# Optimization experiments

Hardware: AMD Instinct MI355X
Metric: run time of the kernel (lower is better)

The kernel has to match this reference:

```python
import math
import jax, jax.numpy as jnp
import numpy as np

L_LAYERS, H, D, DV, DM, LMAX, V = 4, 16, 1024, 64, 4096, 1024, 32000


def setup_inputs() -> dict:
    key = jax.random.key(0)
    ks = iter(jax.random.split(key, 40))
    def rn(shape, s=0.02):
        return jax.random.normal(next(ks), shape, jnp.float32) * s
    x_ids = jax.random.randint(next(ks), (LMAX,), 0, V)
    return dict(
        x_ids=x_ids,
        word_emb=rn((V, D)), pos_emb=rn((LMAX, D)),
        Wq=rn((L_LAYERS, H, D, D)), bq=jnp.zeros((L_LAYERS, H, D), jnp.float32),
        Wk=rn((L_LAYERS, H, D, D)), bk=jnp.zeros((L_LAYERS, H, D), jnp.float32),
        Wv=rn((L_LAYERS, H, D, DV)), bv=jnp.zeros((L_LAYERS, H, DV), jnp.float32),
        Wo=rn((L_LAYERS, H * DV, D)), bo=jnp.zeros((L_LAYERS, D), jnp.float32),
        g1=rn((L_LAYERS, D), 0.01), b1=rn((L_LAYERS, D), 0.01),
        g2=rn((L_LAYERS, D), 0.01), b2=rn((L_LAYERS, D), 0.01),
        W1=rn((L_LAYERS, D, DM)), bm1=jnp.zeros((L_LAYERS, DM), jnp.float32),
        W2=rn((L_LAYERS, DM, D)), bm2=jnp.zeros((L_LAYERS, D), jnp.float32),
        gf=rn((D,), 0.01), bf=rn((D,), 0.01),
        Wu=rn((D, V)), bu=jnp.zeros((V,), jnp.float32),
    )


def _ln(x, g, b):
    # original normalizes each row over the full embedding vector (biased std)
    mu = jnp.mean(x, axis=-1, keepdims=True)
    sd = jnp.sqrt(jnp.mean((x - mu) ** 2, axis=-1, keepdims=True))
    return g * (x - mu) / sd + b


def reference(x_ids, word_emb, pos_emb, Wq, bq, Wk, bk, Wv, bv, Wo, bo,
              g1, b1, g2, b2, W1, bm1, W2, bm2, gf, bf, Wu, bu):
    x = word_emb[x_ids] + pos_emb[jnp.arange(LMAX)]          # (LMAX, D)
    mask = jnp.tril(jnp.ones((LMAX, LMAX), bool))
    scale = 1.0 / math.sqrt(D)                               # d_attn = d_e
    for l in range(L_LAYERS):
        xn = _ln(x, g1[l], b1[l])
        q = jnp.einsum('ld,hde->hle', xn, Wq[l]) + bq[l][:, None, :]
        k = jnp.einsum('ld,hde->hle', xn, Wk[l]) + bk[l][:, None, :]
        v = jnp.einsum('ld,hdv->hlv', xn, Wv[l]) + bv[l][:, None, :]
        s = jnp.einsum('hqe,hke->hqk', q, k)                 # (H, LMAX, LMAX)
        s = jnp.where(mask, s, -jnp.inf)
        a = jax.nn.softmax(s * scale, axis=-1)
        o = jnp.einsum('hqk,hkv->hqv', a, v)                 # (H, LMAX, DV)
        # faithful reproduction of MHAttention's OVERLAPPING slice writes:
        # head h writes columns [h, h+DV), later heads overwrite earlier ones
        y = jnp.zeros((LMAX, H * DV), x.dtype)
        for h in range(H):
            y = y.at[:, h:h + DV].set(o[h])
        x = x + y @ Wo[l] + bo[l]
        xn2 = _ln(x, g2[l], b2[l])
        # x + act_layer(xn2) where act_layer(z) = z + mlp2(gelu(mlp1(z)))
        x = x + xn2 + jax.nn.gelu(xn2 @ W1[l] + bm1[l]) @ W2[l] + bm2[l]
    x = _ln(x, gf, bf)
    return jax.nn.softmax(x @ Wu + bu, axis=-1)              # (LMAX, V)
```

## Files before the change

### kernel.cpp

```cpp
#include <hip/hip_runtime.h>

typedef __bf16 bf16_t;
typedef __bf16 bf16x8 __attribute__((ext_vector_type(8)));
typedef float f32x4 __attribute__((ext_vector_type(4)));
typedef unsigned int u32;

#define SEQ    1024
#define DEMB   1024
#define NHEAD  16
#define DVDIM  64
#define DMLP   4096
#define NVOCAB 32000
#define NLAYER 4

typedef const __attribute__((address_space(1))) void gas_t;
typedef __attribute__((address_space(3))) void las_t;

__device__ __forceinline__ void gload_lds16(const void* g, void* l) {
  __builtin_amdgcn_global_load_lds((gas_t*)g, (las_t*)l, 16, 0, 0);
}

union PackU { bf16_t h[2]; u32 u; };
union B4U  { uint2 u; bf16_t h[4]; };

__device__ __forceinline__ float blockSum(float v, float* red) {
  #pragma unroll
  for (int o = 32; o > 0; o >>= 1) v += __shfl_down(v, o, 64);
  __syncthreads();
  if ((threadIdx.x & 63) == 0) red[threadIdx.x >> 6] = v;
  __syncthreads();
  return (red[0] + red[1]) + (red[2] + red[3]);
}
__device__ __forceinline__ float blockMax(float v, float* red) {
  #pragma unroll
  for (int o = 32; o > 0; o >>= 1) v = fmaxf(v, __shfl_down(v, o, 64));
  __syncthreads();
  if ((threadIdx.x & 63) == 0) red[threadIdx.x >> 6] = v;
  __syncthreads();
  return fmaxf(fmaxf(red[0], red[1]), fmaxf(red[2], red[3]));
}

__device__ __forceinline__ void ln_body(float4 v, const float* __restrict__ g,
                                        const float* __restrict__ b,
                                        bf16_t* __restrict__ xn, int row, int t,
                                        float* red, float* xupd_row) {
  float mu = blockSum(v.x + v.y + v.z + v.w, red) * (1.0f / DEMB);
  float dx = v.x - mu, dy = v.y - mu, dz = v.z - mu, dw = v.w - mu;
  float var = blockSum(dx * dx + dy * dy + dz * dz + dw * dw, red) * (1.0f / DEMB);
  float inv = 1.0f / sqrtf(var);
  float4 gv = *(const float4*)(g + t * 4);
  float4 bv = *(const float4*)(b + t * 4);
  float o0 = gv.x * dx * inv + bv.x;
  float o1 = gv.y * dy * inv + bv.y;
  float o2 = gv.z * dz * inv + bv.z;
  float o3 = gv.w * dw * inv + bv.w;
  PackU p0, p1;
  p0.h[0] = (bf16_t)o0; p0.h[1] = (bf16_t)o1;
  p1.h[0] = (bf16_t)o2; p1.h[1] = (bf16_t)o3;
  uint2 st; st.x = p0.u; st.y = p1.u;
  *(uint2*)(xn + (long)row * DEMB + t * 4) = st;
  if (xupd_row) {
    float4 nv; nv.x = v.x + o0; nv.y = v.y + o1; nv.z = v.z + o2; nv.w = v.w + o3;
    *(float4*)(xupd_row + t * 4) = nv;
  }
}

__global__ void __launch_bounds__(256)
embedln_k(const int* __restrict__ ids, const float* __restrict__ we,
          const float* __restrict__ pe, const float* __restrict__ g,
          const float* __restrict__ b, float* __restrict__ x,
          bf16_t* __restrict__ xn) {
  __shared__ float red[4];
  const int row = blockIdx.x, t = threadIdx.x;
  const long id = ids[row];
  float4 a = *(const float4*)(we + id * (long)DEMB + t * 4);
  float4 p = *(const float4*)(pe + (long)row * DEMB + t * 4);
  float4 v; v.x = a.x + p.x; v.y = a.y + p.y; v.z = a.z + p.z; v.w = a.w + p.w;
  *(float4*)(x + (long)row * DEMB + t * 4) = v;
  ln_body(v, g, b, xn, row, t, red, nullptr);
}

__global__ void __launch_bounds__(256)
ln_k(const float* __restrict__ x, const float* __restrict__ g,
     const float* __restrict__ b, bf16_t* __restrict__ xn,
     float* __restrict__ xupd) {
  __shared__ float red[4];
  const int row = blockIdx.x, t = threadIdx.x;
  float4 v = *(const float4*)(x + (long)row * DEMB + t * 4);
  ln_body(v, g, b, xn, row, t, red, xupd ? xupd + (long)row * DEMB : nullptr);
}

__global__ void __launch_bounds__(256)
redln_k(const float* __restrict__ P, const float* __restrict__ bm2,
        float* __restrict__ X, const float* __restrict__ g,
        const float* __restrict__ b, bf16_t* __restrict__ xn) {
  __shared__ float red[4];
  const int row = blockIdx.x, t = threadIdx.x;
  const long i = (long)row * 1024 + t * 4;
  float4 x = *(float4*)(X + i);
  #pragma unroll
  for (int z = 0; z < 4; ++z) {
    float4 p = *(const float4*)(P + (long)z * 1048576 + i);
    x.x += p.x; x.y += p.y; x.z += p.z; x.w += p.w;
  }
  float4 bb = *(const float4*)(bm2 + t * 4);
  x.x += bb.x; x.y += bb.y; x.z += bb.z; x.w += bb.w;
  *(float4*)(X + i) = x;
  ln_body(x, g, b, xn, row, t, red, nullptr);
}

__global__ void biaszyb_k(const float* __restrict__ bq, const float* __restrict__ bk,
                          float* __restrict__ out, bf16_t* __restrict__ y) {
  const int z = blockIdx.x, t = threadIdx.x;
  if (z < 128) {
    const int l = z >> 5, i = z & 31;
    const float* src = (i < NHEAD) ? (bq + (long)(l * NHEAD + i) * DEMB)
                                   : (bk + (long)(l * NHEAD + i - NHEAD) * DEMB);
    *(float4*)(out + (long)z * DEMB + t * 4) = *(const float4*)(src + t * 4);
  } else {
    *(uint4*)((char*)y + ((long)(z - 128) * 256 + t) * 16) = uint4{0, 0, 0, 0};
  }
}

__device__ __forceinline__ void tconv_tile(const float* __restrict__ ip,
                                           bf16_t* __restrict__ op,
                                           int R, int C, int rx, int ry,
                                           float (*tf)[65]) {
  const int c0 = rx * 64, r0 = ry * 128;
  const int t = threadIdx.x;
  #pragma unroll
  for (int p = 0; p < 8; ++p) {
    const int i = p * 256 + t;
    const int r = i >> 4, c4 = (i & 15) * 4;
    const float4 v = *(const float4*)(ip + (long)(r0 + r) * C + (c0 + c4));
    *(float4*)&tf[r][c4] = v;
  }
  __syncthreads();
  const int nn = t >> 2;
  const int sub = t & 3;
  #pragma unroll
  for (int q2 = 0; q2 < 4; ++q2) {
    const int base = q2 * 32 + sub * 8;
    u32 w[4];
    #pragma unroll
    for (int q = 0; q < 4; ++q) {
      PackU u;
      u.h[0] = (bf16_t)tf[base + 2 * q][nn];
      u.h[1] = (bf16_t)tf[base + 2 * q + 1][nn];
      w[q] = u.u;
    }
    *(uint4*)(op + (long)(c0 + nn) * R + (r0 + base)) = *(uint4*)&w[0];
  }
}

__global__ void __launch_bounds__(256)
tconvall_k(const float* __restrict__ Wq, const float* __restrict__ Wk,
           const float* __restrict__ Wv, const float* __restrict__ Wo,
           const float* __restrict__ W1, const float* __restrict__ W2,
           const float* __restrict__ Wu,
           bf16_t* __restrict__ WTqk, bf16_t* __restrict__ WTv,
           bf16_t* __restrict__ WTo, bf16_t* __restrict__ WT1,
           bf16_t* __restrict__ WT2, bf16_t* __restrict__ WTu) {
  __shared__ float tf[128][65];
  const long DD = (long)DEMB * DEMB;
  const int b = blockIdx.x;
  const float* ip; bf16_t* op; int R, C, rx, ry;
  if (b < 16384) {
    const int z = b >> 7, rem = b & 127; ry = rem >> 4; rx = rem & 15;
    R = 1024; C = 1024;
    const int l = z >> 5, i = z & 31;
    ip = (i < NHEAD) ? (Wq + (long)(l * NHEAD + i) * DD)
                     : (Wk + (long)(l * NHEAD + i - NHEAD) * DD);
    op = WTqk + (long)z * DD;
  } else if (b < 16896) {
    const int idx = b - 16384; const int z = idx >> 3; ry = idx & 7; rx = 0;
    R = 1024; C = 64;
    ip = Wv + (long)z * 65536; op = WTv + (long)z * 65536;
  } else if (b < 16960) {
    const int idx = b - 16896; const int z = idx >> 4; ry = 0; rx = idx & 15;
    R = 128; C = 1024;
    ip = Wo + (long)z * DD; op = WTo + (long)z * 131072;
  } else if (b < 19008) {
    const int idx = b - 16960; const int z = idx >> 9, rem = idx & 511;
    ry = rem >> 6; rx = rem & 63;
    R = 1024; C = 4096;
    ip = W1 + (long)z * 4194304; op = WT1 + (long)z * 4194304;
  } else if (b < 21056) {
    const int idx = b - 19008; const int z = idx >> 9, rem = idx & 511;
    ry = rem >> 4; rx = rem & 15;
    R = 4096; C = 1024;
    ip = W2 + (long)z * 4194304; op = WT2 + (long)z * 4194304;
  } else {
    const int idx = b - 21056; ry = idx / 500; rx = idx - ry * 500;
    R = 1024; C = 32000;
    ip = Wu; op = WTu;
  }
  tconv_tile(ip, op, R, C, rx, ry, tf);
}

template<int MODE, int BN, bool CAUSAL, bool TRIMK>
__global__ void __launch_bounds__(256)
gemm_k(const bf16_t* __restrict__ A, const bf16_t* __restrict__ B,
       const float* __restrict__ bias, void* __restrict__ Cv,
       int M, int N, int K, int lda, int ldb,
       long aB, long bB, long cB, int biasB) {
  __shared__ bf16_t lsA[128 * 32];
  __shared__ bf16_t lsB[BN * 32];

  const int t = threadIdx.x;
  const int bz = blockIdx.z;
  const int m0 = blockIdx.y * 128;
  const int n0 = blockIdx.x * BN;
  if (CAUSAL && n0 > m0 + 127) return;

  const bf16_t* Ap = A + (long)bz * aB;
  const bf16_t* Bp = B + (long)bz * bB;
  const int kEnd = TRIMK ? min(K, m0 + 128) : K;

  constexpr int NS = BN / 32;
  const int lane = t & 63;
  const int wid = t >> 6;
  const int wr = (wid >> 1) * 64;
  const int wc = (wid & 1) * (BN / 2);
  const int fr = lane & 15, fg = lane >> 4;
  const int srow = lane >> 2;
  const int skc  = (lane & 3) * 8;

  f32x4 acc[4][NS] = {};

  for (int k0 = 0; k0 < kEnd; k0 += 32) {
    if (k0) __syncthreads();
    #pragma unroll
    for (int i = 0; i < 2; ++i) {
      const int seg = wid * 2 + i;
      gload_lds16(Ap + (long)(m0 + seg * 16 + srow) * lda + (k0 + skc),
                  lsA + seg * 512);
    }
    if (BN == 128) {
      #pragma unroll
      for (int i = 0; i < 2; ++i) {
        const int seg = wid * 2 + i;
        gload_lds16(Bp + (long)(n0 + seg * 16 + srow) * ldb + (k0 + skc),
                    lsB + seg * 512);
      }
    } else {
      gload_lds16(Bp + (long)(n0 + wid * 16 + srow) * ldb + (k0 + skc),
                  lsB + wid * 512);
    }
    __syncthreads();

    bf16x8 af[4], bfv[NS];
    #pragma unroll
    for (int ms = 0; ms < 4; ++ms)
      af[ms] = *(const bf16x8*)(lsA + (wr + ms * 16 + fr) * 32 + fg * 8);
    #pragma unroll
    for (int ns = 0; ns < NS; ++ns)
      bfv[ns] = *(const bf16x8*)(lsB + (wc + ns * 16 + fr) * 32 + fg * 8);
    #pragma unroll
    for (int ms = 0; ms < 4; ++ms)
      #pragma unroll
      for (int ns = 0; ns < NS; ++ns)
        acc[ms][ns] = __builtin_amdgcn_mfma_f32_16x16x32_bf16(
            af[ms], bfv[ns], acc[ms][ns], 0, 0, 0);
  }

  #pragma unroll
  for (int ms = 0; ms < 4; ++ms) {
    #pragma unroll
    for (int ns = 0; ns < NS; ++ns) {
      const int col = n0 + wc + ns * 16 + fr;
      const float bvv = bias ? bias[(long)bz * biasB + col] : 0.0f;
      #pragma unroll
      for (int r = 0; r < 4; ++r) {
        const int row = m0 + wr + ms * 16 + fg * 4 + r;
        float v = acc[ms][ns][r] + bvv;
        if (MODE == 1) {
          ((float*)Cv)[(long)bz * cB + (long)row * N + col] += v;
        } else if (MODE == 2) {
          ((float*)Cv)[(long)bz * cB + (long)row * N + col] = v;
        } else {
          float gl = 0.5f * v * (1.0f + tanhf(0.7978845608028654f * (v + 0.044715f * v * v * v)));
          ((bf16_t*)Cv)[(long)bz * cB + (long)row * N + col] = (bf16_t)gl;
        }
      }
    }
  }
}

#define GPHASE(buf, mh, nh, STAGE, VM) do {                                            \
  bf16x8 af[4][2], bfv[2][2];                                                          \
  _Pragma("unroll") for (int mf = 0; mf < 4; ++mf) {                                   \
    const int r = wm * 128 + ((mh) * 4 + mf) * 16 + (lane & 15);                       \
    _Pragma("unroll") for (int ks = 0; ks < 2; ++ks) {                                 \
      const int slot = ks * 4 + (lane >> 4);                                           \
      af[mf][ks] = *(const bf16x8*)(lds + (buf) * 32768 + r * 64 +                     \
                                    ((slot ^ (r & 7)) << 3)); } }                      \
  _Pragma("unroll") for (int nf = 0; nf < 2; ++nf) {                                   \
    const int r = wn * 64 + ((nh) * 2 + nf) * 16 + (lane & 15);                        \
    _Pragma("unroll") for (int ks = 0; ks < 2; ++ks) {                                 \
      const int slot = ks * 4 + (lane >> 4);                                           \
      bfv[nf][ks] = *(const bf16x8*)(lds + (buf) * 32768 + 16384 + r * 64 +            \
                                     ((slot ^ (r & 7)) << 3)); } }                     \
  STAGE;                                                                               \
  __builtin_amdgcn_s_barrier();                                                        \
  asm volatile("s_waitcnt lgkmcnt(0)" ::: "memory");                                   \
  __builtin_amdgcn_sched_barrier(0);                                                   \
  __builtin_amdgcn_s_setprio(1);                                                       \
  _Pragma("unroll") for (int mf = 0; mf < 4; ++mf)                                     \
    _Pragma("unroll") for (int nf = 0; nf < 2; ++nf)                                   \
      _Pragma("unroll") for (int ks = 0; ks < 2; ++ks)                                 \
        acc[(mh) * 4 + mf][(nh) * 2 + nf] = __builtin_amdgcn_mfma_f32_16x16x32_bf16(   \
            af[mf][ks], bfv[nf][ks], acc[(mh) * 4 + mf][(nh) * 2 + nf], 0, 0, 0);      \
  __builtin_amdgcn_s_setprio(0);                                                       \
  VM;                                                                                  \
  __builtin_amdgcn_s_barrier();                                                        \
} while (0)

template<int MODE, bool CAUSAL, int VZ, bool PACKED>
__global__ void __launch_bounds__(512, 1)
gemm256_k(const bf16_t* __restrict__ A, const bf16_t* __restrict__ B,
          const float* __restrict__ bias, void* __restrict__ Cv,
          int M, int N, int K, long aB, long bB, long cB, int biasB,
          const bf16_t* __restrict__ A2, const bf16_t* __restrict__ B2,
          const float* __restrict__ bias2, bf16_t* __restrict__ Cv2) {
  __shared__ bf16_t lds[65536];

  const int t = threadIdx.x;
  const int lane = t & 63, w = t >> 6;
  const int wm = w >> 2, wn = w & 3;
  int m0, n0, zz; bool vm;
  if (PACKED) {
    const int id = blockIdx.x;
    if (id < 16) {
      vm = true; zz = 0;
      m0 = (id >> 2) * 256; n0 = (id & 3) * 256;
    } else {
      vm = false;
      const int idd = id - 16;
      zz = idd & 15;
      const int pi = idd >> 4;
      const int by = (pi >= 1) + (pi >= 3) + (pi >= 6);
      const int bx = pi - (by * (by + 1)) / 2;
      m0 = by * 256; n0 = bx * 256;
    }
  } else {
    zz = blockIdx.z; m0 = blockIdx.y * 256; n0 = blockIdx.x * 256;
    vm = (VZ >= 0) && (zz == VZ);
    if (CAUSAL && !vm && n0 > m0 + 255) return;
  }

  const bf16_t* Ap = vm ? A2 : A + (long)zz * aB;
  const bf16_t* Bp = vm ? B2 : B + (long)zz * bB;
  const int NT = K >> 6;

  f32x4 acc[8][4] = {};

  auto stA = [&](int half, int kt, int buf) {
    #pragma unroll
    for (int rr = 0; rr < 2; ++rr) {
      const int rw0 = rr * 64 + w * 8;
      const int row0 = ((rw0 >> 6) << 7) | (half << 6) | (rw0 & 63);
      const int r = row0 + (lane >> 3);
      const int slot = lane & 7;
      gload_lds16(Ap + (long)(m0 + r) * K + (kt << 6) + ((slot ^ (r & 7)) << 3),
                  lds + buf * 32768 + row0 * 64);
    }
  };
  auto stB = [&](int half, int kt, int buf) {
    #pragma unroll
    for (int rr = 0; rr < 2; ++rr) {
      const int rw0 = rr * 64 + w * 8;
      const int row0 = ((rw0 >> 5) << 6) | (half << 5) | (rw0 & 31);
      const int r = row0 + (lane >> 3);
      const int slot = lane & 7;
      gload_lds16(Bp + (long)(n0 + r) * K + (kt << 6) + ((slot ^ (r & 7)) << 3),
                  lds + buf * 32768 + 16384 + row0 * 64);
    }
  };

  stB(0, 0, 0); stA(0, 0, 0); stA(1, 0, 0); stB(1, 0, 0);
  stB(0, 1, 1); stA(0, 1, 1);
  asm volatile("s_waitcnt vmcnt(4)" ::: "memory");
  __builtin_amdgcn_s_barrier();

  for (int it = 0; it < (NT >> 1); ++it) {
    const int tt = it * 2;
    const int s1 = min(tt + 1, NT - 1);
    const int s2 = min(tt + 2, NT - 1);
    const int s3 = min(tt + 3, NT - 1);
    GPHASE(0, 0, 0, { stA(1, s1, 1); }, );
    GPHASE(0, 1, 0, { stB(1, s1, 1); }, );
    GPHASE(0, 0, 1, { stB(0, s2, 0); }, );
    GPHASE(0, 1, 1, { stA(0, s2, 0); }, asm volatile("s_waitcnt vmcnt(4)" ::: "memory"));
    GPHASE(1, 0, 0, { stA(1, s2, 0); }, );
    GPHASE(1, 1, 0, { stB(1, s2, 0); }, );
    GPHASE(1, 0, 1, { stB(0, s3, 1); }, );
    GPHASE(1, 1, 1, { stA(0, s3, 1); }, asm volatile("s_waitcnt vmcnt(4)" ::: "memory"));
  }
  asm volatile("s_waitcnt vmcnt(0)" ::: "memory");

  #pragma unroll
  for (int mf = 0; mf < 8; ++mf) {
    #pragma unroll
    for (int nf = 0; nf < 4; ++nf) {
      const int col = n0 + wn * 64 + nf * 16 + (lane & 15);
      const int row0 = m0 + wm * 128 + mf * 16 + (lane >> 4) * 4;
      if (vm) {
        const float bvv = bias2[col];
        PackU p0, p1;
        p0.h[0] = (bf16_t)(acc[mf][nf][0] + bvv);
        p0.h[1] = (bf16_t)(acc[mf][nf][1] + bvv);
        p1.h[0] = (bf16_t)(acc[mf][nf][2] + bvv);
        p1.h[1] = (bf16_t)(acc[mf][nf][3] + bvv);
        uint2 st; st.x = p0.u; st.y = p1.u;
        *(uint2*)(Cv2 + (long)col * M + row0) = st;
      } else {
        const float bvv = bias ? bias[(long)zz * biasB + col] : 0.0f;
        #pragma unroll
        for (int r = 0; r < 4; ++r) {
          const float v = acc[mf][nf][r] + bvv;
          if (MODE == 0)
            ((bf16_t*)Cv)[(long)zz * cB + (long)(row0 + r) * N + col] = (bf16_t)v;
          else
            ((float*)Cv)[(long)zz * cB + (long)(row0 + r) * N + col] = v;
        }
      }
    }
  }
}

__global__ void __launch_bounds__(256)
smax_k(const bf16_t* __restrict__ s, const bf16_t* __restrict__ V,
       bf16_t* __restrict__ Yb) {
  __shared__ float pl[4][1024];
  const int qb = blockIdx.x, h = blockIdx.y, t = threadIdx.x;
  const int w = t >> 6, lane = t & 63;
  const int q = qb * 4 + w;
  const bf16_t* sr = s + ((long)h * SEQ + q) * SEQ;
  const int L = q + 1;
  const float scale = 0.03125f;
  float e[16];
  float m = -1e30f;
  #pragma unroll
  for (int c = 0; c < 4; ++c) {
    B4U bb; bb.u = *(const uint2*)(sr + lane * 16 + c * 4);
    #pragma unroll
    for (int j = 0; j < 4; ++j) {
      const float x = (float)bb.h[j] * scale;
      e[c * 4 + j] = x;
      if (lane * 16 + c * 4 + j < L) m = fmaxf(m, x);
    }
  }
  #pragma unroll
  for (int o = 32; o > 0; o >>= 1) m = fmaxf(m, __shfl_xor(m, o, 64));
  float sum = 0.0f;
  #pragma unroll
  for (int i = 0; i < 16; ++i) {
    e[i] = (lane * 16 + i < L) ? expf(e[i] - m) : 0.0f;
    sum += e[i];
  }
  #pragma unroll
  for (int o = 32; o > 0; o >>= 1) sum += __shfl_xor(sum, o, 64);
  const float inv = 1.0f / sum;

  if (h != NHEAD - 1) {
    const bf16_t* vc = V + (long)h * 64 * SEQ + lane * 16;
    float d = 0.0f;
    #pragma unroll
    for (int c = 0; c < 4; ++c) {
      B4U vv; vv.u = *(const uint2*)(vc + c * 4);
      #pragma unroll
      for (int j = 0; j < 4; ++j) d += e[c * 4 + j] * (float)vv.h[j];
    }
    #pragma unroll
    for (int o = 32; o > 0; o >>= 1) d += __shfl_xor(d, o, 64);
    if (lane == 0) Yb[(long)q * 128 + h] = (bf16_t)(d * inv);
  } else {
    #pragma unroll
    for (int c = 0; c < 4; ++c)
      *(float4*)&pl[w][lane * 16 + c * 4] = *(float4*)&e[c * 4];
    __syncthreads();
    const int c = t & 63, r = t >> 6;
    const int qq = qb * 4 + r;
    const bf16_t* vr = V + ((long)(NHEAD - 1) * 64 + c) * SEQ;
    float d = 0.0f;
    for (int kk = 0; kk < 1024; kk += 8) {
      bf16x8 v8 = *(const bf16x8*)(vr + kk);
      #pragma unroll
      for (int j = 0; j < 8; ++j) d += pl[r][kk + j] * (float)v8[j];
    }
    float sr2 = 0.0f;
    for (int kk = t & 63; kk < 1024; kk += 64) sr2 += pl[r][kk];
    #pragma unroll
    for (int o = 32; o > 0; o >>= 1) sr2 += __shfl_xor(sr2, o, 64);
    Yb[(long)qq * 128 + 15 + c] = (bf16_t)(d / sr2);
  }
}

__global__ void __launch_bounds__(1024)
vsmax_k(float* __restrict__ out) {
  __shared__ float rm[16], rs[16];
  const int row = blockIdx.x, t = threadIdx.x;
  float* r = out + (long)row * NVOCAB;
  float v[32];
  const int nlast = (t < NVOCAB - 31 * 1024) ? 32 : 31;
  float m = -1e30f;
  #pragma unroll
  for (int j = 0; j < 31; ++j) { v[j] = r[j * 1024 + t]; m = fmaxf(m, v[j]); }
  if (nlast == 32) { v[31] = r[31 * 1024 + t]; m = fmaxf(m, v[31]); } else v[31] = -1e30f;
  float s = 0.0f;
  #pragma unroll
  for (int j = 0; j < 32; ++j) s += expf(v[j] - m);
  #pragma unroll
  for (int o = 32; o > 0; o >>= 1) {
    const float mo = __shfl_down(m, o, 64);
    const float so = __shfl_down(s, o, 64);
    const float M2 = fmaxf(m, mo);
    s = s * expf(m - M2) + so * expf(mo - M2);
    m = M2;
  }
  if ((t & 63) == 0) { rm[t >> 6] = m; rs[t >> 6] = s; }
  __syncthreads();
  float M = -1e30f;
  #pragma unroll
  for (int i = 0; i < 16; ++i) M = fmaxf(M, rm[i]);
  float S = 0.0f;
  #pragma unroll
  for (int i = 0; i < 16; ++i) S += rs[i] * expf(rm[i] - M);
  const float inv = 1.0f / S;
  #pragma unroll
  for (int j = 0; j < 31; ++j) r[j * 1024 + t] = expf(v[j] - M) * inv;
  if (nlast == 32) r[31 * 1024 + t] = expf(v[31] - M) * inv;
}

extern "C" void kernel_launch(void* const* d_in, const int* in_sizes, int n_in,
                              void* d_out, int out_size, void* d_ws, size_t ws_size,
                              hipStream_t stream) {
  (void)in_sizes; (void)n_in; (void)out_size; (void)ws_size;
  const int*   x_ids = (const int*)  d_in[0];
  const float* wemb  = (const float*)d_in[1];
  const float* pemb  = (const float*)d_in[2];
  const float* Wq    = (const float*)d_in[3];
  const float* bq    = (const float*)d_in[4];
  const float* Wk    = (const float*)d_in[5];
  const float* bk    = (const float*)d_in[6];
  const float* Wv    = (const float*)d_in[7];
  const float* bv    = (const float*)d_in[8];
  const float* Wo    = (const float*)d_in[9];
  const float* bo    = (const float*)d_in[10];
  const float* g1    = (const float*)d_in[11];
  const float* b1    = (const float*)d_in[12];
  const float* g2    = (const float*)d_in[13];
  const float* b2    = (const float*)d_in[14];
  const float* W1    = (const float*)d_in[15];
  const float* bm1   = (const float*)d_in[16];
  const float* W2    = (const float*)d_in[17];
  const float* bm2   = (const float*)d_in[18];
  const float* gf    = (const float*)d_in[19];
  const float* bfin  = (const float*)d_in[20];
  const float* Wu    = (const float*)d_in[21];
  const float* bu    = (const float*)d_in[22];

  char* ws = (char*)d_ws;
  float*  X    = (float*) ws;
  bf16_t* ACT  = (bf16_t*)(ws + (4u   << 20));
  bf16_t* VbT  = (bf16_t*)(ws + (6u   << 20));
  bf16_t* Yb   = (bf16_t*)(ws + (10u  << 20));
  bf16_t* H1   = (bf16_t*)(ws + (12u  << 20));
  bf16_t* QKb  = (bf16_t*)(ws + (20u  << 20));
  float*  PART = (float*) (ws + (84u  << 20));
  float*  BIAS = (float*) (ws + (100u << 20));
  bf16_t* WTqk = (bf16_t*)(ws + (128u << 20));
  bf16_t* WTv  = (bf16_t*)(ws + (384u << 20));
  bf16_t* WTo  = (bf16_t*)(ws + (392u << 20));
  bf16_t* WT1  = (bf16_t*)(ws + (400u << 20));
  bf16_t* WT2  = (bf16_t*)(ws + (432u << 20));
  bf16_t* WTu  = (bf16_t*)(ws + (464u << 20));

  bf16_t* Sb  = (bf16_t*)d_out;
  float*  OUT = (float*)d_out;

  const long DD = (long)DEMB * DEMB;
  const long SD = (long)SEQ * DEMB;

  embedln_k<<<SEQ, 256, 0, stream>>>(x_ids, wemb, pemb, g1, b1, X, ACT);
  biaszyb_k<<<192, 256, 0, stream>>>(bq, bk, BIAS, Yb);
  tconvall_k<<<25056, 256, 0, stream>>>(Wq, Wk, Wv, Wo, W1, W2, Wu,
                                        WTqk, WTv, WTo, WT1, WT2, WTu);

  for (int l = 0; l < NLAYER; ++l) {
    gemm256_k<0, false, -1, false><<<dim3(4, 4, 32), 512, 0, stream>>>(
        ACT, WTqk + (long)l * 32 * DD, BIAS + (long)l * 32 * DEMB, QKb,
        SEQ, DEMB, DEMB, 0L, DD, SD, DEMB,
        nullptr, nullptr, nullptr, nullptr);

    gemm256_k<0, true, 0, true><<<dim3(176), 512, 0, stream>>>(
        QKb, QKb + (long)NHEAD * SD, nullptr, Sb,
        SEQ, SEQ, DEMB, SD, SD, (long)SEQ * SEQ, 0,
        ACT, WTv + (long)l * DD, bv + (long)l * NHEAD * DVDIM, VbT);

    smax_k<<<dim3(SEQ / 4, NHEAD), 256, 0, stream>>>(Sb, VbT, Yb);

    gemm_k<1, 64, false, false><<<dim3(16, 8, 1), 256, 0, stream>>>(
        Yb, WTo + (long)l * DEMB * 128, bo + (long)l * DEMB, X,
        SEQ, DEMB, 128, 128, 128, 0L, 0L, 0L, 0);

    ln_k<<<SEQ, 256, 0, stream>>>(X, g2 + l * DEMB, b2 + l * DEMB, ACT, X);

    gemm_k<3, 128, false, false><<<dim3(32, 8, 1), 256, 0, stream>>>(
        ACT, WT1 + (long)l * DMLP * DEMB, bm1 + (long)l * DMLP, H1,
        SEQ, DMLP, DEMB, DEMB, DEMB, 0L, 0L, 0L, 0);
    gemm_k<2, 128, false, false><<<dim3(8, 8, 4), 256, 0, stream>>>(
        H1, WT2 + (long)l * DEMB * DMLP, nullptr, PART,
        SEQ, DEMB, 1024, DMLP, DMLP, 1024L, 1024L, (long)SEQ * DEMB, 0);
    if (l < NLAYER - 1)
      redln_k<<<SEQ, 256, 0, stream>>>(PART, bm2 + (long)l * DEMB, X,
                                       g1 + (l + 1) * DEMB, b1 + (l + 1) * DEMB, ACT);
    else
      redln_k<<<SEQ, 256, 0, stream>>>(PART, bm2 + (long)l * DEMB, X, gf, bfin, ACT);
  }

  gemm256_k<2, false, -1, false><<<dim3(125, 4, 1), 512, 0, stream>>>(
      ACT, WTu, bu, OUT, SEQ, NVOCAB, DEMB, 0L, 0L, 0L, 0,
      nullptr, nullptr, nullptr, nullptr);
  vsmax_k<<<SEQ, 1024, 0, stream>>>(OUT);
}
```

Baseline: 1.393 ms.

## Write bf16 logits to workspace, fuse init kernels, nontemporal weight-transpose stores

The vocab GEMM now writes bf16 logits into a scratch region (reusing the QK weight area) instead of fp32 into the output. The softmax kernel reads these bf16 pairs and writes fp32 probabilities as float2, which halves the logit write and read traffic. The embedding/LN kernel absorbs the bias-copy and zero-fill kernel, saving one launch. Weight-transpose stores become nontemporal. Rounding logits to bf16 before the softmax adds precision error.

```diff
diff --git a/kernel.cpp b/kernel.cpp
--- a/kernel.cpp
+++ b/kernel.cpp
@@ -4,6 +4,7 @@
 typedef __bf16 bf16x8 __attribute__((ext_vector_type(8)));
 typedef float f32x4 __attribute__((ext_vector_type(4)));
 typedef unsigned int u32;
+typedef u32 u32x4 __attribute__((ext_vector_type(4)));
 
 #define SEQ    1024
 #define DEMB   1024
@@ -30,14 +31,6 @@
   if ((threadIdx.x & 63) == 0) red[threadIdx.x >> 6] = v;
   __syncthreads();
   return (red[0] + red[1]) + (red[2] + red[3]);
-}
-__device__ __forceinline__ float blockMax(float v, float* red) {
-  #pragma unroll
-  for (int o = 32; o > 0; o >>= 1) v = fmaxf(v, __shfl_down(v, o, 64));
-  __syncthreads();
-  if ((threadIdx.x & 63) == 0) red[threadIdx.x >> 6] = v;
-  __syncthreads();
-  return fmaxf(fmaxf(red[0], red[1]), fmaxf(red[2], red[3]));
 }
 
 __device__ __forceinline__ void ln_body(float4 v, const float* __restrict__ g,
@@ -66,18 +59,32 @@
 }
 
 __global__ void __launch_bounds__(256)
-embedln_k(const int* __restrict__ ids, const float* __restrict__ we,
-          const float* __restrict__ pe, const float* __restrict__ g,
-          const float* __restrict__ b, float* __restrict__ x,
-          bf16_t* __restrict__ xn) {
+embedlnbias_k(const int* __restrict__ ids, const float* __restrict__ we,
+              const float* __restrict__ pe, const float* __restrict__ g,
+              const float* __restrict__ b, float* __restrict__ x,
+              bf16_t* __restrict__ xn,
+              const float* __restrict__ bq, const float* __restrict__ bk,
+              float* __restrict__ bias_out, bf16_t* __restrict__ y) {
   __shared__ float red[4];
-  const int row = blockIdx.x, t = threadIdx.x;
-  const long id = ids[row];
-  float4 a = *(const float4*)(we + id * (long)DEMB + t * 4);
-  float4 p = *(const float4*)(pe + (long)row * DEMB + t * 4);
-  float4 v; v.x = a.x + p.x; v.y = a.y + p.y; v.z = a.z + p.z; v.w = a.w + p.w;
-  *(float4*)(x + (long)row * DEMB + t * 4) = v;
-  ln_body(v, g, b, xn, row, t, red, nullptr);
+  const int bidx = blockIdx.x, t = threadIdx.x;
+  if (bidx < SEQ) {
+    const int row = bidx;
+    const long id = ids[row];
+    float4 a = *(const float4*)(we + id * (long)DEMB + t * 4);
+    float4 p = *(const float4*)(pe + (long)row * DEMB + t * 4);
+    float4 v; v.x = a.x + p.x; v.y = a.y + p.y; v.z = a.z + p.z; v.w = a.w + p.w;
+    *(float4*)(x + (long)row * DEMB + t * 4) = v;
+    ln_body(v, g, b, xn, row, t, red, nullptr);
+  } else if (bidx < SEQ + 128) {
+    const int z = bidx - SEQ;
+    const int l = z >> 5, i = z & 31;
+    const float* src = (i < NHEAD) ? (bq + (long)(l * NHEAD + i) * DEMB)
+                                   : (bk + (long)(l * NHEAD + i - NHEAD) * DEMB);
+    *(float4*)(bias_out + (long)z * DEMB + t * 4) = *(const float4*)(src + t * 4);
+  } else {
+    const int z = bidx - SEQ - 128;
+    *(uint4*)((char*)y + ((long)z * 256 + t) * 16) = uint4{0, 0, 0, 0};
+  }
 }
 
 __global__ void __launch_bounds__(256)
@@ -109,19 +116,6 @@
   ln_body(x, g, b, xn, row, t, red, nullptr);
 }
 
-__global__ void biaszyb_k(const float* __restrict__ bq, const float* __restrict__ bk,
-                          float* __restrict__ out, bf16_t* __restrict__ y) {
-  const int z = blockIdx.x, t = threadIdx.x;
-  if (z < 128) {
-    const int l = z >> 5, i = z & 31;
-    const float* src = (i < NHEAD) ? (bq + (long)(l * NHEAD + i) * DEMB)
-                                   : (bk + (long)(l * NHEAD + i - NHEAD) * DEMB);
-    *(float4*)(out + (long)z * DEMB + t * 4) = *(const float4*)(src + t * 4);
-  } else {
-    *(uint4*)((char*)y + ((long)(z - 128) * 256 + t) * 16) = uint4{0, 0, 0, 0};
-  }
-}
-
 __device__ __forceinline__ void tconv_tile(const float* __restrict__ ip,
                                            bf16_t* __restrict__ op,
                                            int R, int C, int rx, int ry,
@@ -141,7 +135,7 @@
   #pragma unroll
   for (int q2 = 0; q2 < 4; ++q2) {
     const int base = q2 * 32 + sub * 8;
-    u32 w[4];
+    u32x4 w;
     #pragma unroll
     for (int q = 0; q < 4; ++q) {
       PackU u;
@@ -149,7 +143,8 @@
       u.h[1] = (bf16_t)tf[base + 2 * q + 1][nn];
       w[q] = u.u;
     }
-    *(uint4*)(op + (long)(c0 + nn) * R + (r0 + base)) = *(uint4*)&w[0];
+    __builtin_nontemporal_store(w,
+        (u32x4*)(op + (long)(c0 + nn) * R + (r0 + base)));
   }
 }
 
@@ -498,16 +493,25 @@
 }
 
 __global__ void __launch_bounds__(1024)
-vsmax_k(float* __restrict__ out) {
+vsmax_k(const bf16_t* __restrict__ lg, float* __restrict__ out) {
   __shared__ float rm[16], rs[16];
   const int row = blockIdx.x, t = threadIdx.x;
+  const bf16_t* lr = lg + (long)row * NVOCAB;
   float* r = out + (long)row * NVOCAB;
   float v[32];
-  const int nlast = (t < NVOCAB - 31 * 1024) ? 32 : 31;
   float m = -1e30f;
   #pragma unroll
-  for (int j = 0; j < 31; ++j) { v[j] = r[j * 1024 + t]; m = fmaxf(m, v[j]); }
-  if (nlast == 32) { v[31] = r[31 * 1024 + t]; m = fmaxf(m, v[31]); } else v[31] = -1e30f;
+  for (int j = 0; j < 16; ++j) {
+    const int c = 2 * (j * 1024 + t);
+    if (j < 15 || t < 640) {
+      PackU u; u.u = *(const u32*)(lr + c);
+      v[2 * j]     = (float)u.h[0];
+      v[2 * j + 1] = (float)u.h[1];
+      m = fmaxf(m, fmaxf(v[2 * j], v[2 * j + 1]));
+    } else {
+      v[2 * j] = v[2 * j + 1] = -1e30f;
+    }
+  }
   float s = 0.0f;
   #pragma unroll
   for (int j = 0; j < 32; ++j) s += expf(v[j] - m);
@@ -529,8 +533,13 @@
   for (int i = 0; i < 16; ++i) S += rs[i] * expf(rm[i] - M);
   const float inv = 1.0f / S;
   #pragma unroll
-  for (int j = 0; j < 31; ++j) r[j * 1024 + t] = expf(v[j] - M) * inv;
-  if (nlast == 32) r[31 * 1024 + t] = expf(v[31] - M) * inv;
+  for (int j = 0; j < 16; ++j) {
+    const int c = 2 * (j * 1024 + t);
+    if (j < 15 || t < 640) {
+      float2 p; p.x = expf(v[2 * j] - M) * inv; p.y = expf(v[2 * j + 1] - M) * inv;
+      *(float2*)(r + c) = p;
+    }
+  }
 }
 
 extern "C" void kernel_launch(void* const* d_in, const int* in_sizes, int n_in,
@@ -571,6 +580,7 @@
   float*  PART = (float*) (ws + (84u  << 20));
   float*  BIAS = (float*) (ws + (100u << 20));
   bf16_t* WTqk = (bf16_t*)(ws + (128u << 20));
+  bf16_t* LOGIT= (bf16_t*)(ws + (128u << 20));
   bf16_t* WTv  = (bf16_t*)(ws + (384u << 20));
   bf16_t* WTo  = (bf16_t*)(ws + (392u << 20));
   bf16_t* WT1  = (bf16_t*)(ws + (400u << 20));
@@ -583,8 +593,8 @@
   const long DD = (long)DEMB * DEMB;
   const long SD = (long)SEQ * DEMB;
 
-  embedln_k<<<SEQ, 256, 0, stream>>>(x_ids, wemb, pemb, g1, b1, X, ACT);
-  biaszyb_k<<<192, 256, 0, stream>>>(bq, bk, BIAS, Yb);
+  embedlnbias_k<<<SEQ + 128 + 64, 256, 0, stream>>>(
+      x_ids, wemb, pemb, g1, b1, X, ACT, bq, bk, BIAS, Yb);
   tconvall_k<<<25056, 256, 0, stream>>>(Wq, Wk, Wv, Wo, W1, W2, Wu,
                                         WTqk, WTv, WTo, WT1, WT2, WTu);
 
@@ -620,8 +630,8 @@
       redln_k<<<SEQ, 256, 0, stream>>>(PART, bm2 + (long)l * DEMB, X, gf, bfin, ACT);
   }
 
-  gemm256_k<2, false, -1, false><<<dim3(125, 4, 1), 512, 0, stream>>>(
-      ACT, WTu, bu, OUT, SEQ, NVOCAB, DEMB, 0L, 0L, 0L, 0,
+  gemm256_k<0, false, -1, false><<<dim3(125, 4, 1), 512, 0, stream>>>(
+      ACT, WTu, bu, LOGIT, SEQ, NVOCAB, DEMB, 0L, 0L, 0L, 0,
       nullptr, nullptr, nullptr, nullptr);
-  vsmax_k<<<SEQ, 1024, 0, stream>>>(OUT);
-}
+  vsmax_k<<<SEQ, 1024, 0, stream>>>(LOGIT, OUT);
+}
```

Measured after the change: 1.398 ms. About the same (+0.4%).
